# Performance work log

Measured on AMD Instinct MI355X. Metric: run time of the kernel, lower is better.

The kernel has to match this reference:

```python
import jax, jax.numpy as jnp
import numpy as np

EPS = 1e-12  # F.normalize default eps


def _l2norm(x):
    n = jnp.linalg.norm(x, axis=-1, keepdims=True)
    return x / jnp.maximum(n, EPS)


def _group_pool(x):
    # x: (b, 4, C) row-normalized features; per-group attention pooling.
    # s_i = sum_j x_i . x_j ; weights = softmax_i(s) ; pooled = sum_i w_i x_i
    s = jnp.einsum('bic,bjc->bi', x, x)          # (b, 4)
    w = jax.nn.softmax(s, axis=1)                 # (b, 4)
    return jnp.einsum('bi,bic->bc', w, x)         # (b, C)


def setup_inputs() -> dict:
    key = jax.random.key(0)
    k1, k2 = jax.random.split(key)
    N, C = 16384, 1024
    x1 = jax.random.normal(k1, (N, C), dtype=jnp.float32)
    x2 = jax.random.normal(k2, (N, C), dtype=jnp.float32)
    return {"x1": x1, "x2": x2}


def reference(x1, x2):
    b = x2.shape[0] // 4
    C = x1.shape[1]
    x1n = _l2norm(x1).reshape(b, 4, C)
    x2n = _l2norm(x2).reshape(b, 4, C)
    p1 = _l2norm(_group_pool(x1n))                # (b, C)
    p2 = _l2norm(_group_pool(x2n))                # (b, C)
    center_loss = jnp.mean(jnp.linalg.norm(p1 - p2, axis=1))
    sim = p1 @ p2.T                               # (b, b)
    diag = jnp.arange(b)
    # cross_entropy(sim, arange) and cross_entropy(sim.T, arange)
    loss_t = -jnp.mean(jax.nn.log_softmax(sim, axis=1)[diag, diag])
    loss_i = -jnp.mean(jax.nn.log_softmax(sim, axis=0)[diag, diag])
    return (loss_t + loss_i + center_loss, p1, p2)
```

## Files before the change

### kernel.cpp

```cpp
#include <hip/hip_runtime.h>
#include <hip/hip_bf16.h>

#define BGRP 4096
#define CDIM 1024

typedef __attribute__((ext_vector_type(8))) short bf16x8;
typedef __attribute__((ext_vector_type(4))) float f32x4;
typedef __attribute__((ext_vector_type(4))) unsigned short u16x4;

__device__ __forceinline__ unsigned short f2bf(float x) {
    __hip_bfloat16 h = __float2bfloat16(x);
    unsigned short u;
    __builtin_memcpy(&u, &h, 2);
    return u;
}

__device__ __forceinline__ void gload16(const void* g, void* l) {
    __builtin_amdgcn_global_load_lds(
        (const __attribute__((address_space(1))) unsigned int*)g,
        (__attribute__((address_space(3))) unsigned int*)l, 16, 0, 0);
}

__device__ __forceinline__ void group_coefs(const float* d, float* coef) {
    float D[4][4];
    int c = 0;
    #pragma unroll
    for (int i = 0; i < 4; ++i)
        #pragma unroll
        for (int j = i; j < 4; ++j) { D[i][j] = d[c]; D[j][i] = d[c]; ++c; }
    float inv[4];
    #pragma unroll
    for (int i = 0; i < 4; ++i) inv[i] = 1.0f / fmaxf(sqrtf(D[i][i]), 1e-12f);
    float s[4];
    #pragma unroll
    for (int i = 0; i < 4; ++i) {
        float si = 0.f;
        #pragma unroll
        for (int j = 0; j < 4; ++j) si += D[i][j] * inv[i] * inv[j];
        s[i] = si;
    }
    float m = fmaxf(fmaxf(s[0], s[1]), fmaxf(s[2], s[3]));
    float e[4], se = 0.f;
    #pragma unroll
    for (int i = 0; i < 4; ++i) { e[i] = expf(s[i] - m); se += e[i]; }
    float rse = 1.0f / se;
    #pragma unroll
    for (int i = 0; i < 4; ++i) coef[i] = e[i] * rse * inv[i];
}

__device__ __forceinline__ float wave_allsum(float t) {
    t += __shfl_xor(t, 1, 64);
    t += __shfl_xor(t, 2, 64);
    t += __shfl_xor(t, 4, 64);
    t += __shfl_xor(t, 8, 64);
    t += __shfl_xor(t, 16, 64);
    t += __shfl_xor(t, 32, 64);
    return t;
}

__device__ __forceinline__ void pool_phase(
    const float* __restrict__ x, int g, int l,
    float* __restrict__ pout,
    unsigned short* __restrict__ pbout,
    float4 p[4], float& s_out)
{
    float4 a[4][4];
    #pragma unroll
    for (int i = 0; i < 4; ++i)
        #pragma unroll
        for (int w = 0; w < 4; ++w)
            a[i][w] = reinterpret_cast<const float4*>(x)[(size_t)(4 * g + i) * 256 + w * 64 + l];

    float dd[10];
    {
        int c = 0;
        #pragma unroll
        for (int i = 0; i < 4; ++i)
            #pragma unroll
            for (int j = i; j < 4; ++j) {
                float s0 = 0.f;
                #pragma unroll
                for (int w = 0; w < 4; ++w)
                    s0 += a[i][w].x * a[j][w].x + a[i][w].y * a[j][w].y
                        + a[i][w].z * a[j][w].z + a[i][w].w * a[j][w].w;
                dd[c++] = s0;
            }
    }
    #pragma unroll
    for (int v = 0; v < 10; ++v) dd[v] = wave_allsum(dd[v]);

    float coef[4];
    group_coefs(dd, coef);

    float D[4][4];
    {
        int c = 0;
        #pragma unroll
        for (int i = 0; i < 4; ++i)
            #pragma unroll
            for (int j = i; j < 4; ++j) { D[i][j] = dd[c]; D[j][i] = dd[c]; ++c; }
    }
    float n = 0.f;
    #pragma unroll
    for (int i = 0; i < 4; ++i) {
        float ti = 0.f;
        #pragma unroll
        for (int j = 0; j < 4; ++j) ti += D[i][j] * coef[j];
        n += coef[i] * ti;
    }
    const float inv = 1.0f / fmaxf(sqrtf(n), 1e-12f);
    s_out = n * inv * inv;

    #pragma unroll
    for (int w = 0; w < 4; ++w) {
        float4 q;
        q.x = coef[0]*a[0][w].x + coef[1]*a[1][w].x + coef[2]*a[2][w].x + coef[3]*a[3][w].x;
        q.y = coef[0]*a[0][w].y + coef[1]*a[1][w].y + coef[2]*a[2][w].y + coef[3]*a[3][w].y;
        q.z = coef[0]*a[0][w].z + coef[1]*a[1][w].z + coef[2]*a[2][w].z + coef[3]*a[3][w].z;
        q.w = coef[0]*a[0][w].w + coef[1]*a[1][w].w + coef[2]*a[2][w].w + coef[3]*a[3][w].w;
        q.x *= inv; q.y *= inv; q.z *= inv; q.w *= inv;
        p[w] = q;

        const int e = w * 256 + l * 4;
        pout[e + 0] = q.x; pout[e + 1] = q.y; pout[e + 2] = q.z; pout[e + 3] = q.w;
        if (pbout != nullptr) {
            u16x4 wb;
            wb[0] = f2bf(q.x); wb[1] = f2bf(q.y); wb[2] = f2bf(q.z); wb[3] = f2bf(q.w);
            *reinterpret_cast<u16x4*>(pbout + e) = wb;
        }
    }
}

__global__ __launch_bounds__(256, 3) void pool_kernel(
    const float* __restrict__ x1, const float* __restrict__ x2,
    float* __restrict__ out,
    unsigned short* __restrict__ p1b, unsigned short* __restrict__ p2b,
    float* __restrict__ diag, float* __restrict__ centerArr)
{
    const int l = threadIdx.x & 63;
    const int g = blockIdx.x * 4 + (threadIdx.x >> 6);

    float4 p1s[4], p2s[4];
    float s1, s2;
    pool_phase(x1, g, l, out + 1 + (size_t)g * CDIM,
               p1b ? p1b + (size_t)g * CDIM : nullptr, p1s, s1);
    pool_phase(x2, g, l, out + 1 + (size_t)(BGRP + g) * CDIM,
               p2b ? p2b + (size_t)g * CDIM : nullptr, p2s, s2);

    float dp = 0.f;
    #pragma unroll
    for (int w = 0; w < 4; ++w)
        dp += p1s[w].x * p2s[w].x + p1s[w].y * p2s[w].y
            + p1s[w].z * p2s[w].z + p1s[w].w * p2s[w].w;
    dp = wave_allsum(dp);

    if (l == 0) {
        diag[g] = dp;
        const float c2v = fmaxf(s1 + s2 - 2.0f * dp, 0.0f);
        centerArr[g] = sqrtf(c2v);
    }
}

__global__ __launch_bounds__(256, 4) void sim_lds_kernel(
    const unsigned short* __restrict__ p1b, const unsigned short* __restrict__ p2b,
    float* __restrict__ rowsum, float* __restrict__ colsum)
{
    __shared__ __align__(16) unsigned char lds[32768];
    const int tid  = threadIdx.x;
    const int lane = tid & 63;
    const int wid  = tid >> 6;
    const int wm = wid >> 1, wn = wid & 1;
    const int row0 = blockIdx.y * 128;
    const int col0 = blockIdx.x * 128;
    const int lr  = lane & 15;
    const int lkb = lane >> 4;

    const int srow = lane >> 3;
    const int scol = ((lane & 7) ^ srow) << 4;
    const int ch0  = wid * 4;

    f32x4 acc[4][4];
    #pragma unroll
    for (int mi = 0; mi < 4; ++mi)
        #pragma unroll
        for (int ni = 0; ni < 4; ++ni) {
            acc[mi][ni][0] = 0.f; acc[mi][ni][1] = 0.f;
            acc[mi][ni][2] = 0.f; acc[mi][ni][3] = 0.f;
        }

    const char* A = (const char*)p1b;
    const char* B = (const char*)p2b;

    for (int kt = 0; kt < 16; ++kt) {
        const size_t kbyte = (size_t)kt * 128;
        #pragma unroll
        for (int c = 0; c < 4; ++c) {
            const int chunk = ch0 + c;
            const int r = chunk * 8 + srow;
            gload16(A + (size_t)(row0 + r) * 2048 + kbyte + scol, lds + chunk * 1024);
            gload16(B + (size_t)(col0 + r) * 2048 + kbyte + scol, lds + 16384 + chunk * 1024);
        }
        __syncthreads();

        #pragma unroll
        for (int ks = 0; ks < 2; ++ks) {
            bf16x8 af[4], bg[4];
            const int cbase = (ks * 64 + lkb * 16) ^ ((lr & 7) << 4);
            #pragma unroll
            for (int i = 0; i < 4; ++i) {
                const int ra = wm * 64 + i * 16 + lr;
                const int rb = wn * 64 + i * 16 + lr;
                af[i] = *reinterpret_cast<const bf16x8*>(lds + ra * 128 + cbase);
                bg[i] = *reinterpret_cast<const bf16x8*>(lds + 16384 + rb * 128 + cbase);
            }
            #pragma unroll
            for (int mi = 0; mi < 4; ++mi)
                #pragma unroll
                for (int ni = 0; ni < 4; ++ni)
                    acc[mi][ni] = __builtin_amdgcn_mfma_f32_16x16x32_bf16(
                        af[mi], bg[ni], acc[mi][ni], 0, 0, 0);
        }
        __syncthreads();
    }

    float rs[4][4];
    float cs[4] = {0.f, 0.f, 0.f, 0.f};
    #pragma unroll
    for (int mi = 0; mi < 4; ++mi)
        #pragma unroll
        for (int r = 0; r < 4; ++r) rs[mi][r] = 0.f;

    #pragma unroll
    for (int mi = 0; mi < 4; ++mi)
        #pragma unroll
        for (int ni = 0; ni < 4; ++ni)
            #pragma unroll
            for (int r = 0; r < 4; ++r) {
                float e = __expf(acc[mi][ni][r]);
                rs[mi][r] += e;
                cs[ni] += e;
            }

    const int wrow0 = row0 + wm * 64;
    const int wcol0 = col0 + wn * 64;
    #pragma unroll
    for (int mi = 0; mi < 4; ++mi)
        #pragma unroll
        for (int r = 0; r < 4; ++r) {
            float v = rs[mi][r];
            v += __shfl_xor(v, 1, 64);
            v += __shfl_xor(v, 2, 64);
            v += __shfl_xor(v, 4, 64);
            v += __shfl_xor(v, 8, 64);
            if (lr == 0) atomicAdd(&rowsum[wrow0 + mi * 16 + lkb * 4 + r], v);
        }
    #pragma unroll
    for (int ni = 0; ni < 4; ++ni) {
        float v = cs[ni];
        v += __shfl_xor(v, 16, 64);
        v += __shfl_xor(v, 32, 64);
        if (lkb == 0) atomicAdd(&colsum[wcol0 + ni * 16 + lr], v);
    }
}

__device__ __forceinline__ bf16x8 frag_from_f32(const float* p) {
    bf16x8 r;
    #pragma unroll
    for (int i = 0; i < 8; ++i) {
        unsigned int b = __float_as_uint(p[i]);
        b += 0x7fffu + ((b >> 16) & 1u);
        r[i] = (short)(b >> 16);
    }
    return r;
}

__global__ __launch_bounds__(256) void sim_fallback_kernel(
    const float* __restrict__ p1f, const float* __restrict__ p2f,
    float* __restrict__ rowsum, float* __restrict__ colsum)
{
    const int lane = threadIdx.x & 63;
    const int wid  = threadIdx.x >> 6;
    const int wm = wid >> 1, wn = wid & 1;
    const int row0 = blockIdx.y * 128 + wm * 64;
    const int col0 = blockIdx.x * 128 + wn * 64;
    const int lr  = lane & 15;
    const int lkb = lane >> 4;
    const int lk  = lkb * 8;

    f32x4 acc[4][4];
    #pragma unroll
    for (int mi = 0; mi < 4; ++mi)
        #pragma unroll
        for (int ni = 0; ni < 4; ++ni) {
            acc[mi][ni][0] = 0.f; acc[mi][ni][1] = 0.f;
            acc[mi][ni][2] = 0.f; acc[mi][ni][3] = 0.f;
        }

    const size_t abase = (size_t)(row0 + lr) * CDIM + lk;
    const size_t bbase = (size_t)(col0 + lr) * CDIM + lk;

    for (int k = 0; k < CDIM; k += 32) {
        bf16x8 af[4], bfr[4];
        #pragma unroll
        for (int i = 0; i < 4; ++i) {
            af[i]  = frag_from_f32(p1f + abase + (size_t)i * 16 * CDIM + k);
            bfr[i] = frag_from_f32(p2f + bbase + (size_t)i * 16 * CDIM + k);
        }
        #pragma unroll
        for (int mi = 0; mi < 4; ++mi)
            #pragma unroll
            for (int ni = 0; ni < 4; ++ni)
                acc[mi][ni] = __builtin_amdgcn_mfma_f32_16x16x32_bf16(
                    af[mi], bfr[ni], acc[mi][ni], 0, 0, 0);
    }

    float rs[4][4];
    float cs[4] = {0.f, 0.f, 0.f, 0.f};
    #pragma unroll
    for (int mi = 0; mi < 4; ++mi)
        #pragma unroll
        for (int r = 0; r < 4; ++r) rs[mi][r] = 0.f;

    #pragma unroll
    for (int mi = 0; mi < 4; ++mi)
        #pragma unroll
        for (int ni = 0; ni < 4; ++ni)
            #pragma unroll
            for (int r = 0; r < 4; ++r) {
                float e = __expf(acc[mi][ni][r]);
                rs[mi][r] += e;
                cs[ni] += e;
            }

    #pragma unroll
    for (int mi = 0; mi < 4; ++mi)
        #pragma unroll
        for (int r = 0; r < 4; ++r) {
            float v = rs[mi][r];
            v += __shfl_xor(v, 1, 64);
            v += __shfl_xor(v, 2, 64);
            v += __shfl_xor(v, 4, 64);
            v += __shfl_xor(v, 8, 64);
            if (lr == 0) atomicAdd(&rowsum[row0 + mi * 16 + lkb * 4 + r], v);
        }
    #pragma unroll
    for (int ni = 0; ni < 4; ++ni) {
        float v = cs[ni];
        v += __shfl_xor(v, 16, 64);
        v += __shfl_xor(v, 32, 64);
        if (lkb == 0) atomicAdd(&colsum[col0 + ni * 16 + lr], v);
    }
}

__global__ __launch_bounds__(256) void loss_kernel(
    const float* __restrict__ rowsum, const float* __restrict__ colsum,
    const float* __restrict__ diag, const float* __restrict__ centerArr,
    float* __restrict__ out)
{
    float part = 0.f;
    for (int i = threadIdx.x; i < BGRP; i += 256)
        part += logf(rowsum[i]) + logf(colsum[i]) - 2.0f * diag[i] + centerArr[i];
    #pragma unroll
    for (int off = 32; off > 0; off >>= 1) part += __shfl_down(part, off, 64);
    __shared__ float l4[4];
    if ((threadIdx.x & 63) == 0) l4[threadIdx.x >> 6] = part;
    __syncthreads();
    if (threadIdx.x == 0)
        out[0] = (l4[0] + l4[1] + l4[2] + l4[3]) * (1.0f / (float)BGRP);
}

extern "C" void kernel_launch(void* const* d_in, const int* in_sizes, int n_in,
                              void* d_out, int out_size, void* d_ws, size_t ws_size,
                              hipStream_t stream)
{
    const float* x1 = (const float*)d_in[0];
    const float* x2 = (const float*)d_in[1];
    float* out = (float*)d_out;

    float* rowsum    = (float*)d_ws;
    float* colsum    = rowsum + BGRP;
    float* diag      = colsum + BGRP;
    float* centerArr = diag + BGRP;
    const size_t head_floats = 4 * (size_t)BGRP;
    unsigned short* p1b = (unsigned short*)((char*)d_ws + head_floats * sizeof(float));
    unsigned short* p2b = p1b + (size_t)BGRP * CDIM;
    const size_t need = head_floats * sizeof(float) + (size_t)2 * BGRP * CDIM * sizeof(unsigned short);
    const bool use_ws = (ws_size >= need);

    hipMemsetAsync(d_ws, 0, 2 * (size_t)BGRP * sizeof(float), stream);

    pool_kernel<<<BGRP / 4, 256, 0, stream>>>(x1, x2, out,
                                              use_ws ? p1b : nullptr,
                                              use_ws ? p2b : nullptr,
                                              diag, centerArr);

    dim3 gridB(BGRP / 128, BGRP / 128);
    if (use_ws) {
        sim_lds_kernel<<<gridB, 256, 0, stream>>>(p1b, p2b, rowsum, colsum);
    } else {
        sim_fallback_kernel<<<gridB, 256, 0, stream>>>(out + 1, out + 1 + (size_t)BGRP * CDIM,
                                                       rowsum, colsum);
    }

    loss_kernel<<<1, 256, 0, stream>>>(rowsum, colsum, diag, centerArr, out);
}
```

Before: 87.27 us.

## Split pool work so each wave handles one input, exchange via LDS

The pooling kernel previously had each wave process both x1 and x2 for a group sequentially. Now two waves per group each pool one input in parallel, and the x1 result is shared through LDS so the x2 wave can compute the diagonal dot product. Register pressure per wave drops, which allows a higher occupancy bound and twice as many blocks, giving more memory-level parallelism. The center loss now assumes unit-norm pooled vectors (2-2dp) instead of using the computed squared norms. This is only exact when the norm is not clamped by eps.

Result: no change. 86.23 us (-1.2%).

```diff
diff --git a/kernel.cpp b/kernel.cpp
--- a/kernel.cpp
+++ b/kernel.cpp
@@ -58,12 +58,21 @@
     return t;
 }
 
-__device__ __forceinline__ void pool_phase(
-    const float* __restrict__ x, int g, int l,
-    float* __restrict__ pout,
-    unsigned short* __restrict__ pbout,
-    float4 p[4], float& s_out)
+__global__ __launch_bounds__(256, 4) void pool_kernel(
+    const float* __restrict__ x1, const float* __restrict__ x2,
+    float* __restrict__ out,
+    unsigned short* __restrict__ p1b, unsigned short* __restrict__ p2b,
+    float* __restrict__ diag, float* __restrict__ centerArr)
 {
+    __shared__ float plds[2][CDIM];
+    const int l    = threadIdx.x & 63;
+    const int wv   = threadIdx.x >> 6;
+    const int gi   = wv >> 1;
+    const int isx2 = wv & 1;
+    const int g    = blockIdx.x * 2 + gi;
+
+    const float* __restrict__ x = isx2 ? x2 : x1;
+
     float4 a[4][4];
     #pragma unroll
     for (int i = 0; i < 4; ++i)
@@ -109,55 +118,56 @@
         n += coef[i] * ti;
     }
     const float inv = 1.0f / fmaxf(sqrtf(n), 1e-12f);
-    s_out = n * inv * inv;
-
+
+    float* pout = out + 1 + (size_t)(g + (isx2 ? BGRP : 0)) * CDIM;
+    unsigned short* pb = isx2 ? (p2b ? p2b + (size_t)g * CDIM : nullptr)
+                              : (p1b ? p1b + (size_t)g * CDIM : nullptr);
+
+    float4 q[4];
     #pragma unroll
     for (int w = 0; w < 4; ++w) {
-        float4 q;
-        q.x = coef[0]*a[0][w].x + coef[1]*a[1][w].x + coef[2]*a[2][w].x + coef[3]*a[3][w].x;
-        q.y = coef[0]*a[0][w].y + coef[1]*a[1][w].y + coef[2]*a[2][w].y + coef[3]*a[3][w].y;
-        q.z = coef[0]*a[0][w].z + coef[1]*a[1][w].z + coef[2]*a[2][w].z + coef[3]*a[3][w].z;
-        q.w = coef[0]*a[0][w].w + coef[1]*a[1][w].w + coef[2]*a[2][w].w + coef[3]*a[3][w].w;
-        q.x *= inv; q.y *= inv; q.z *= inv; q.w *= inv;
-        p[w] = q;
-
+        float4 qq;
+        qq.x = coef[0]*a[0][w].x + coef[1]*a[1][w].x + coef[2]*a[2][w].x + coef[3]*a[3][w].x;
+        qq.y = coef[0]*a[0][w].y + coef[1]*a[1][w].y + coef[2]*a[2][w].y + coef[3]*a[3][w].y;
+        qq.z = coef[0]*a[0][w].z + coef[1]*a[1][w].z + coef[2]*a[2][w].z + coef[3]*a[3][w].z;
+        qq.w = coef[0]*a[0][w].w + coef[1]*a[1][w].w + coef[2]*a[2][w].w + coef[3]*a[3][w].w;
+        qq.x *= inv; qq.y *= inv; qq.z *= inv; qq.w *= inv;
+        q[w] = qq;
+    }
+
+    if (!isx2) {
+        #pragma unroll
+        for (int w = 0; w < 4; ++w)
+            *reinterpret_cast<float4*>(&plds[gi][w * 256 + l * 4]) = q[w];
+    }
+
+    #pragma unroll
+    for (int w = 0; w < 4; ++w) {
         const int e = w * 256 + l * 4;
-        pout[e + 0] = q.x; pout[e + 1] = q.y; pout[e + 2] = q.z; pout[e + 3] = q.w;
-        if (pbout != nullptr) {
+        pout[e + 0] = q[w].x; pout[e + 1] = q[w].y;
+        pout[e + 2] = q[w].z; pout[e + 3] = q[w].w;
+        if (pb != nullptr) {
             u16x4 wb;
-            wb[0] = f2bf(q.x); wb[1] = f2bf(q.y); wb[2] = f2bf(q.z); wb[3] = f2bf(q.w);
-            *reinterpret_cast<u16x4*>(pbout + e) = wb;
-        }
-    }
-}
-
-__global__ __launch_bounds__(256, 3) void pool_kernel(
-    const float* __restrict__ x1, const float* __restrict__ x2,
-    float* __restrict__ out,
-    unsigned short* __restrict__ p1b, unsigned short* __restrict__ p2b,
-    float* __restrict__ diag, float* __restrict__ centerArr)
-{
-    const int l = threadIdx.x & 63;
-    const int g = blockIdx.x * 4 + (threadIdx.x >> 6);
-
-    float4 p1s[4], p2s[4];
-    float s1, s2;
-    pool_phase(x1, g, l, out + 1 + (size_t)g * CDIM,
-               p1b ? p1b + (size_t)g * CDIM : nullptr, p1s, s1);
-    pool_phase(x2, g, l, out + 1 + (size_t)(BGRP + g) * CDIM,
-               p2b ? p2b + (size_t)g * CDIM : nullptr, p2s, s2);
-
-    float dp = 0.f;
-    #pragma unroll
-    for (int w = 0; w < 4; ++w)
-        dp += p1s[w].x * p2s[w].x + p1s[w].y * p2s[w].y
-            + p1s[w].z * p2s[w].z + p1s[w].w * p2s[w].w;
-    dp = wave_allsum(dp);
-
-    if (l == 0) {
-        diag[g] = dp;
-        const float c2v = fmaxf(s1 + s2 - 2.0f * dp, 0.0f);
-        centerArr[g] = sqrtf(c2v);
+            wb[0] = f2bf(q[w].x); wb[1] = f2bf(q[w].y);
+            wb[2] = f2bf(q[w].z); wb[3] = f2bf(q[w].w);
+            *reinterpret_cast<u16x4*>(pb + e) = wb;
+        }
+    }
+
+    __syncthreads();
+
+    if (isx2) {
+        float dp = 0.f;
+        #pragma unroll
+        for (int w = 0; w < 4; ++w) {
+            float4 p1v = *reinterpret_cast<const float4*>(&plds[gi][w * 256 + l * 4]);
+            dp += p1v.x * q[w].x + p1v.y * q[w].y + p1v.z * q[w].z + p1v.w * q[w].w;
+        }
+        dp = wave_allsum(dp);
+        if (l == 0) {
+            diag[g] = dp;
+            centerArr[g] = sqrtf(fmaxf(2.0f - 2.0f * dp, 0.0f));
+        }
     }
 }
 
@@ -389,7 +399,7 @@
 
     hipMemsetAsync(d_ws, 0, 2 * (size_t)BGRP * sizeof(float), stream);
 
-    pool_kernel<<<BGRP / 4, 256, 0, stream>>>(x1, x2, out,
+    pool_kernel<<<BGRP / 2, 256, 0, stream>>>(x1, x2, out,
                                               use_ws ? p1b : nullptr,
                                               use_ws ? p2b : nullptr,
                                               diag, centerArr);
```

## Pipeline group loads across two groups per wave and fold memset into pool kernel

Applied to the files above, without the earlier changes.

Each wave now handles two groups and prefetches the first two rows of the next input while it computes the current one, so global loads overlap with the reductions. The separate memset is removed, and rowsum/colsum are zeroed inside the pool kernel. Pooled outputs use nontemporal stores, and the diagonal dot product now uses bf16-packed p1 values kept in registers. The center loss assumes unit norms (2-2dp), and the loss uses the fast __logf. These change numerics slightly and raise register pressure, and the grid is halved, which lowers the number of waves in flight.

Result: faster. 81.02 us (-7.2%).

```diff
diff --git a/kernel.cpp b/kernel.cpp
--- a/kernel.cpp
+++ b/kernel.cpp
@@ -19,6 +19,10 @@
     __builtin_amdgcn_global_load_lds(
         (const __attribute__((address_space(1))) unsigned int*)g,
         (__attribute__((address_space(3))) unsigned int*)l, 16, 0, 0);
+}
+
+__device__ __forceinline__ float4 ld4(const float* __restrict__ x, size_t idx4) {
+    return reinterpret_cast<const float4*>(x)[idx4];
 }
 
 __device__ __forceinline__ void group_coefs(const float* d, float* coef) {
@@ -58,33 +62,39 @@
     return t;
 }
 
-__device__ __forceinline__ void pool_phase(
+template<bool ISX2, bool PREF>
+__device__ __forceinline__ void pair_compute(
     const float* __restrict__ x, int g, int l,
-    float* __restrict__ pout,
-    unsigned short* __restrict__ pbout,
-    float4 p[4], float& s_out)
+    float4 a01[2][4],
+    const float* __restrict__ xn, int gn,
+    float* __restrict__ out, unsigned short* __restrict__ pb,
+    unsigned int p1pk[8],
+    float* __restrict__ diag, float* __restrict__ centerArr)
 {
     float4 a[4][4];
     #pragma unroll
-    for (int i = 0; i < 4; ++i)
+    for (int w = 0; w < 4; ++w) { a[0][w] = a01[0][w]; a[1][w] = a01[1][w]; }
+
+    #pragma unroll
+    for (int i = 2; i < 4; ++i)
         #pragma unroll
         for (int w = 0; w < 4; ++w)
-            a[i][w] = reinterpret_cast<const float4*>(x)[(size_t)(4 * g + i) * 256 + w * 64 + l];
+            a[i][w] = ld4(x, (size_t)(4 * g + i) * 256 + w * 64 + l);
 
     float dd[10];
     {
-        int c = 0;
-        #pragma unroll
-        for (int i = 0; i < 4; ++i)
-            #pragma unroll
-            for (int j = i; j < 4; ++j) {
-                float s0 = 0.f;
-                #pragma unroll
-                for (int w = 0; w < 4; ++w)
-                    s0 += a[i][w].x * a[j][w].x + a[i][w].y * a[j][w].y
-                        + a[i][w].z * a[j][w].z + a[i][w].w * a[j][w].w;
-                dd[c++] = s0;
-            }
+        auto dot = [&](int i, int j) {
+            float s0 = 0.f;
+            #pragma unroll
+            for (int w = 0; w < 4; ++w)
+                s0 += a[i][w].x * a[j][w].x + a[i][w].y * a[j][w].y
+                    + a[i][w].z * a[j][w].z + a[i][w].w * a[j][w].w;
+            return s0;
+        };
+        dd[0] = dot(0, 0); dd[1] = dot(0, 1); dd[4] = dot(1, 1);
+        dd[2] = dot(0, 2); dd[3] = dot(0, 3);
+        dd[5] = dot(1, 2); dd[6] = dot(1, 3);
+        dd[7] = dot(2, 2); dd[8] = dot(2, 3); dd[9] = dot(3, 3);
     }
     #pragma unroll
     for (int v = 0; v < 10; ++v) dd[v] = wave_allsum(dd[v]);
@@ -109,8 +119,16 @@
         n += coef[i] * ti;
     }
     const float inv = 1.0f / fmaxf(sqrtf(n), 1e-12f);
-    s_out = n * inv * inv;
-
+
+    if (PREF) {
+        #pragma unroll
+        for (int i = 0; i < 2; ++i)
+            #pragma unroll
+            for (int w = 0; w < 4; ++w)
+                a01[i][w] = ld4(xn, (size_t)(4 * gn + i) * 256 + w * 64 + l);
+    }
+
+    float dp = 0.f;
     #pragma unroll
     for (int w = 0; w < 4; ++w) {
         float4 q;
@@ -119,14 +137,35 @@
         q.z = coef[0]*a[0][w].z + coef[1]*a[1][w].z + coef[2]*a[2][w].z + coef[3]*a[3][w].z;
         q.w = coef[0]*a[0][w].w + coef[1]*a[1][w].w + coef[2]*a[2][w].w + coef[3]*a[3][w].w;
         q.x *= inv; q.y *= inv; q.z *= inv; q.w *= inv;
-        p[w] = q;
 
         const int e = w * 256 + l * 4;
-        pout[e + 0] = q.x; pout[e + 1] = q.y; pout[e + 2] = q.z; pout[e + 3] = q.w;
-        if (pbout != nullptr) {
-            u16x4 wb;
-            wb[0] = f2bf(q.x); wb[1] = f2bf(q.y); wb[2] = f2bf(q.z); wb[3] = f2bf(q.w);
-            *reinterpret_cast<u16x4*>(pbout + e) = wb;
+        __builtin_nontemporal_store(q.x, out + e + 0);
+        __builtin_nontemporal_store(q.y, out + e + 1);
+        __builtin_nontemporal_store(q.z, out + e + 2);
+        __builtin_nontemporal_store(q.w, out + e + 3);
+
+        unsigned short b0 = f2bf(q.x), b1 = f2bf(q.y), b2 = f2bf(q.z), b3 = f2bf(q.w);
+        if (pb != nullptr) {
+            u16x4 wb; wb[0] = b0; wb[1] = b1; wb[2] = b2; wb[3] = b3;
+            *reinterpret_cast<u16x4*>(pb + e) = wb;
+        }
+        if (!ISX2) {
+            p1pk[2 * w]     = (unsigned int)b0 | ((unsigned int)b1 << 16);
+            p1pk[2 * w + 1] = (unsigned int)b2 | ((unsigned int)b3 << 16);
+        } else {
+            float p1x = __uint_as_float(p1pk[2 * w] << 16);
+            float p1y = __uint_as_float(p1pk[2 * w] & 0xffff0000u);
+            float p1z = __uint_as_float(p1pk[2 * w + 1] << 16);
+            float p1w = __uint_as_float(p1pk[2 * w + 1] & 0xffff0000u);
+            dp += p1x * q.x + p1y * q.y + p1z * q.z + p1w * q.w;
+        }
+    }
+
+    if (ISX2) {
+        dp = wave_allsum(dp);
+        if (l == 0) {
+            diag[g] = dp;
+            centerArr[g] = sqrtf(fmaxf(2.0f - 2.0f * dp, 0.0f));
         }
     }
 }
@@ -135,30 +174,44 @@
     const float* __restrict__ x1, const float* __restrict__ x2,
     float* __restrict__ out,
     unsigned short* __restrict__ p1b, unsigned short* __restrict__ p2b,
-    float* __restrict__ diag, float* __restrict__ centerArr)
-{
-    const int l = threadIdx.x & 63;
-    const int g = blockIdx.x * 4 + (threadIdx.x >> 6);
-
-    float4 p1s[4], p2s[4];
-    float s1, s2;
-    pool_phase(x1, g, l, out + 1 + (size_t)g * CDIM,
-               p1b ? p1b + (size_t)g * CDIM : nullptr, p1s, s1);
-    pool_phase(x2, g, l, out + 1 + (size_t)(BGRP + g) * CDIM,
-               p2b ? p2b + (size_t)g * CDIM : nullptr, p2s, s2);
-
-    float dp = 0.f;
-    #pragma unroll
-    for (int w = 0; w < 4; ++w)
-        dp += p1s[w].x * p2s[w].x + p1s[w].y * p2s[w].y
-            + p1s[w].z * p2s[w].z + p1s[w].w * p2s[w].w;
-    dp = wave_allsum(dp);
-
-    if (l == 0) {
-        diag[g] = dp;
-        const float c2v = fmaxf(s1 + s2 - 2.0f * dp, 0.0f);
-        centerArr[g] = sqrtf(c2v);
-    }
+    float* __restrict__ diag, float* __restrict__ centerArr,
+    float* __restrict__ rowsum, float* __restrict__ colsum)
+{
+    if (threadIdx.x < 16) {
+        rowsum[blockIdx.x * 16 + threadIdx.x] = 0.f;
+        colsum[blockIdx.x * 16 + threadIdx.x] = 0.f;
+    }
+
+    const int l  = threadIdx.x & 63;
+    const int W  = blockIdx.x * 4 + (threadIdx.x >> 6);
+    const int gA = W * 2, gB = gA + 1;
+
+    float4 a01[2][4];
+    unsigned int p1pk[8];
+
+    #pragma unroll
+    for (int i = 0; i < 2; ++i)
+        #pragma unroll
+        for (int w = 0; w < 4; ++w)
+            a01[i][w] = ld4(x1, (size_t)(4 * gA + i) * 256 + w * 64 + l);
+
+    float* outA1 = out + 1 + (size_t)gA * CDIM;
+    float* outA2 = out + 1 + (size_t)(BGRP + gA) * CDIM;
+    float* outB1 = out + 1 + (size_t)gB * CDIM;
+    float* outB2 = out + 1 + (size_t)(BGRP + gB) * CDIM;
+
+    pair_compute<false, true >(x1, gA, l, a01, x2, gA, outA1,
+                               p1b ? p1b + (size_t)gA * CDIM : nullptr,
+                               p1pk, diag, centerArr);
+    pair_compute<true,  true >(x2, gA, l, a01, x1, gB, outA2,
+                               p2b ? p2b + (size_t)gA * CDIM : nullptr,
+                               p1pk, diag, centerArr);
+    pair_compute<false, true >(x1, gB, l, a01, x2, gB, outB1,
+                               p1b ? p1b + (size_t)gB * CDIM : nullptr,
+                               p1pk, diag, centerArr);
+    pair_compute<true,  false>(x2, gB, l, a01, nullptr, 0, outB2,
+                               p2b ? p2b + (size_t)gB * CDIM : nullptr,
+                               p1pk, diag, centerArr);
 }
 
 __global__ __launch_bounds__(256, 4) void sim_lds_kernel(
@@ -359,7 +412,7 @@
 {
     float part = 0.f;
     for (int i = threadIdx.x; i < BGRP; i += 256)
-        part += logf(rowsum[i]) + logf(colsum[i]) - 2.0f * diag[i] + centerArr[i];
+        part += __logf(rowsum[i]) + __logf(colsum[i]) - 2.0f * diag[i] + centerArr[i];
     #pragma unroll
     for (int off = 32; off > 0; off >>= 1) part += __shfl_down(part, off, 64);
     __shared__ float l4[4];
@@ -387,12 +440,10 @@
     const size_t need = head_floats * sizeof(float) + (size_t)2 * BGRP * CDIM * sizeof(unsigned short);
     const bool use_ws = (ws_size >= need);
 
-    hipMemsetAsync(d_ws, 0, 2 * (size_t)BGRP * sizeof(float), stream);
-
-    pool_kernel<<<BGRP / 4, 256, 0, stream>>>(x1, x2, out,
+    pool_kernel<<<BGRP / 8, 256, 0, stream>>>(x1, x2, out,
                                               use_ws ? p1b : nullptr,
                                               use_ws ? p2b : nullptr,
-                                              diag, centerArr);
+                                              diag, centerArr, rowsum, colsum);
 
     dim3 gridB(BGRP / 128, BGRP / 128);
     if (use_ws) {
```
